# Kernel optimization log

Measured on AMD Instinct MI355X. Metric: run time of the kernel, lower is better.

## Reference

```python
import jax, jax.numpy as jnp
import numpy as np

B, C, H, W = 8, 320, 64, 64
NUM_SAMPLES = 3


def _skew(v):
    z = jnp.zeros((), v.dtype)
    return jnp.stack([
        jnp.stack([z, -v[2], v[1]]),
        jnp.stack([v[2], z, -v[0]]),
        jnp.stack([-v[1], v[0], z]),
    ])


def _rodrigues(rv):
    theta = jnp.linalg.norm(rv)
    r = rv / jnp.maximum(theta, 1e-12)
    I = jnp.eye(3, dtype=rv.dtype)
    R = jnp.cos(theta) * I + (1 - jnp.cos(theta)) * jnp.outer(r, r) + jnp.sin(theta) * _skew(r)
    return jnp.where(theta < 1e-6, I, R)


def _fundamental(Ks, Kt, ps, pt):
    Rs = jax.vmap(_rodrigues)(ps[:, :3])
    Rt = jax.vmap(_rodrigues)(pt[:, :3])
    ts, tt = ps[:, 3:], pt[:, 3:]
    R_rel = jnp.einsum('bij,bkj->bik', Rs, Rt)          # R_s @ R_t^T
    t_rel = ts - jnp.einsum('bij,bj->bi', R_rel, tt)
    E = jnp.einsum('bij,bjk->bik', jax.vmap(_skew)(t_rel), R_rel)
    inv_Ks = jnp.linalg.inv(Ks)
    inv_Kt = jnp.linalg.inv(Kt)
    return jnp.einsum('bji,bjk,bkl->bil', inv_Kt, E, inv_Ks)  # inv(Kt)^T @ E @ inv(Ks)


def _epipolar_warp(x, Ks, Kt, ps, pt, conv_w, conv_b):
    Bs, Cc, Hh, Ww = x.shape
    Fm = _fundamental(Ks, Kt, ps, pt)
    # pixel homogeneous coords, row-major flatten; H==W makes torch's i*H+j
    # loop index identical to this flat order
    k = jnp.arange(Hh * Ww)
    px = (k % Ww).astype(x.dtype)
    py = (k // Ww).astype(x.dtype)
    P = jnp.stack([px, py, jnp.ones_like(px)])            # [3, HW]
    lines = jnp.einsum('bji,jn->bin', Fm, P)              # F^T @ P -> [B,3,HW]
    a, b, c = lines[:, 0], lines[:, 1], lines[:, 2]
    W1, H1 = float(Ww - 1), float(Hh - 1)
    EPS = 1e-10
    x1 = jnp.clip(-c / (a + EPS), 0.0, W1)
    x2 = jnp.clip(-(b * H1 + c) / (a + EPS), 0.0, W1)
    y1 = jnp.clip(-c / (b + EPS), 0.0, H1)
    y2 = jnp.clip(-(a * W1 + c) / (b + EPS), 0.0, H1)
    t = jnp.linspace(0.0, 1.0, NUM_SAMPLES, dtype=x.dtype)
    sx = (x1[..., None] * (1 - t) + x2[..., None] * t).reshape(Bs, -1)  # [B, HW*3]
    sy = (y1[..., None] * (1 - t) + y2[..., None] * t).reshape(Bs, -1)
    # bilinear sampling; grid_sample(align_corners=True) normalization round-trips
    # back to pixel coords, and all samples are in-bounds by construction
    x0 = jnp.floor(sx)
    y0 = jnp.floor(sy)
    wx = sx - x0
    wy = sy - y0
    x0i = jnp.clip(x0, 0, Ww - 1).astype(jnp.int32)
    x1i = jnp.clip(x0 + 1, 0, Ww - 1).astype(jnp.int32)
    y0i = jnp.clip(y0, 0, Hh - 1).astype(jnp.int32)
    y1i = jnp.clip(y0 + 1, 0, Hh - 1).astype(jnp.int32)
    flat = x.reshape(Bs, Cc, Hh * Ww)

    def gather(yi, xi):
        return jnp.take_along_axis(flat, (yi * Ww + xi)[:, None, :], axis=2)  # [B,C,HW*3]

    g00, g10 = gather(y0i, x0i), gather(y0i, x1i)
    g01, g11 = gather(y1i, x0i), gather(y1i, x1i)
    wx_, wy_ = wx[:, None], wy[:, None]
    val = (g00 * (1 - wx_) * (1 - wy_) + g10 * wx_ * (1 - wy_)
           + g01 * (1 - wx_) * wy_ + g11 * wx_ * wy_)
    sampled = val.reshape(Bs, Cc, Hh * Ww, NUM_SAMPLES).mean(-1).reshape(Bs, Cc, Hh, Ww)
    out = jax.lax.conv_general_dilated(sampled, conv_w, (1, 1), 'SAME',
                                       dimension_numbers=('NCHW', 'OIHW', 'NCHW'))
    out = out + conv_b[None, :, None, None]
    return jax.nn.relu(out)


def setup_inputs() -> dict:
    key = jax.random.key(0)
    ks = jax.random.split(key, 8)
    x = jax.random.normal(ks[0], (B, C, H, W), dtype=jnp.float32)

    def make_K(kk):
        f = jax.random.uniform(kk, (B,), minval=400.0, maxval=600.0, dtype=jnp.float32)
        K = jnp.zeros((B, 3, 3), jnp.float32)
        K = K.at[:, 0, 0].set(f).at[:, 1, 1].set(f)
        K = K.at[:, 0, 2].set(W / 2.0).at[:, 1, 2].set(H / 2.0).at[:, 2, 2].set(1.0)
        return K

    source_intrinsics = make_K(ks[1])
    target_intrinsics = make_K(ks[2])
    source_pose = jnp.concatenate([
        0.3 * jax.random.normal(ks[3], (B, 3), jnp.float32),
        jax.random.normal(ks[4], (B, 3), jnp.float32)], axis=1)
    target_pose = jnp.concatenate([
        0.3 * jax.random.normal(ks[5], (B, 3), jnp.float32),
        jax.random.normal(ks[6], (B, 3), jnp.float32)], axis=1)
    fan_in = C * 3 * 3
    conv_w = jax.random.normal(ks[7], (C, C, 3, 3), jnp.float32) / np.sqrt(fan_in)
    conv_b = jnp.zeros((C,), jnp.float32)
    return {"x": x, "source_intrinsics": source_intrinsics,
            "target_intrinsics": target_intrinsics, "source_pose": source_pose,
            "target_pose": target_pose, "conv_w": conv_w, "conv_b": conv_b}


def reference(x, source_intrinsics, target_intrinsics, source_pose, target_pose, conv_w, conv_b):
    return _epipolar_warp(x, source_intrinsics, target_intrinsics,
                          source_pose, target_pose, conv_w, conv_b)
```

## Files before the change

kernel.cpp:

```cpp
#include <hip/hip_runtime.h>
#include <math.h>

#define BATCH 8
#define CH 320
#define HW 4096

typedef unsigned short u16;
typedef __attribute__((ext_vector_type(8))) short bf16x8;
typedef __attribute__((ext_vector_type(8))) unsigned short u16x8;
typedef __attribute__((ext_vector_type(4))) float f32x4;
typedef __attribute__((ext_vector_type(4))) float float4v;

#define ZP_OFF 0
#define SAMP_OFF 788480
#define WT_OFF 21760000

#define IBUF_BYTES 17408
#define A_OFF (2*IBUF_BYTES)
#define APHASE 61440
#define LDS_TOTAL (A_OFF + 2*APHASE)

__device__ __forceinline__ u16 f2bf(float f) {
    union { float f; unsigned u; } v; v.f = f;
    unsigned r = v.u + 0x7fffu + ((v.u >> 16) & 1u);
    return (u16)(r >> 16);
}
__device__ __forceinline__ float bf2f(u16 h) {
    union { unsigned u; float f; } v; v.u = ((unsigned)h) << 16;
    return v.f;
}
__device__ __forceinline__ void gl_lds16(const void* g, void* l) {
    __builtin_amdgcn_global_load_lds(
        (const __attribute__((address_space(1))) unsigned*)g,
        (__attribute__((address_space(3))) unsigned*)l, 16, 0, 0);
}

__device__ __forceinline__ void rodrigues3(float rv0, float rv1, float rv2, float* R) {
    float theta = sqrtf(rv0*rv0 + rv1*rv1 + rv2*rv2);
    float it = 1.0f / fmaxf(theta, 1e-12f);
    float r0 = rv0*it, r1 = rv1*it, r2 = rv2*it;
    float c = cosf(theta), s = sinf(theta), o = 1.0f - c;
    R[0]=c+o*r0*r0;    R[1]=o*r0*r1-s*r2; R[2]=o*r0*r2+s*r1;
    R[3]=o*r1*r0+s*r2; R[4]=c+o*r1*r1;    R[5]=o*r1*r2-s*r0;
    R[6]=o*r2*r0-s*r1; R[7]=o*r2*r1+s*r0; R[8]=c+o*r2*r2;
    if (theta < 1e-6f) { R[0]=1;R[1]=0;R[2]=0;R[3]=0;R[4]=1;R[5]=0;R[6]=0;R[7]=0;R[8]=1; }
}

__device__ __forceinline__ void inv3(const float* M, float* o) {
    float a=M[0],b=M[1],c=M[2],d=M[3],e=M[4],f=M[5],g=M[6],h=M[7],i=M[8];
    float A = e*i - f*h, B = f*g - d*i, C = d*h - e*g;
    float id = 1.0f / (a*A + b*B + c*C);
    o[0]=A*id;         o[1]=(c*h-b*i)*id; o[2]=(b*f-c*e)*id;
    o[3]=B*id;         o[4]=(a*i-c*g)*id; o[5]=(c*d-a*f)*id;
    o[6]=C*id;         o[7]=(b*g-a*h)*id; o[8]=(a*e-b*d)*id;
}

__device__ void compute_F(const float* Ks, const float* Kt, const float* ps,
                          const float* pt, int b, float* Fm) {
    float Rs[9], Rt[9];
    rodrigues3(ps[b*6+0], ps[b*6+1], ps[b*6+2], Rs);
    rodrigues3(pt[b*6+0], pt[b*6+1], pt[b*6+2], Rt);
    float Rr[9];
    #pragma unroll
    for (int i = 0; i < 3; ++i)
      #pragma unroll
      for (int k = 0; k < 3; ++k)
        Rr[i*3+k] = Rs[i*3+0]*Rt[k*3+0] + Rs[i*3+1]*Rt[k*3+1] + Rs[i*3+2]*Rt[k*3+2];
    float tt0 = pt[b*6+3], tt1 = pt[b*6+4], tt2 = pt[b*6+5];
    float tr0 = ps[b*6+3] - (Rr[0]*tt0 + Rr[1]*tt1 + Rr[2]*tt2);
    float tr1 = ps[b*6+4] - (Rr[3]*tt0 + Rr[4]*tt1 + Rr[5]*tt2);
    float tr2 = ps[b*6+5] - (Rr[6]*tt0 + Rr[7]*tt1 + Rr[8]*tt2);
    float E[9];
    #pragma unroll
    for (int j = 0; j < 3; ++j) {
        E[0*3+j] = -tr2*Rr[1*3+j] + tr1*Rr[2*3+j];
        E[1*3+j] =  tr2*Rr[0*3+j] - tr0*Rr[2*3+j];
        E[2*3+j] = -tr1*Rr[0*3+j] + tr0*Rr[1*3+j];
    }
    float iKs[9], iKt[9];
    inv3(Ks + b*9, iKs);
    inv3(Kt + b*9, iKt);
    float T[9];
    #pragma unroll
    for (int i = 0; i < 3; ++i)
      #pragma unroll
      for (int k = 0; k < 3; ++k)
        T[i*3+k] = iKt[0*3+i]*E[0*3+k] + iKt[1*3+i]*E[1*3+k] + iKt[2*3+i]*E[2*3+k];
    #pragma unroll
    for (int i = 0; i < 3; ++i)
      #pragma unroll
      for (int l = 0; l < 3; ++l)
        Fm[i*3 + l] = T[i*3+0]*iKs[0*3+l] + T[i*3+1]*iKs[1*3+l] + T[i*3+2]*iKs[2*3+l];
}

#define PLIDX(p) (((p)<<3) ^ (((p)&0x70)>>1))

__global__ __launch_bounds__(512) void k_sample8(const float* __restrict__ x,
                                                 const float* __restrict__ Ks,
                                                 const float* __restrict__ Kt,
                                                 const float* __restrict__ ps,
                                                 const float* __restrict__ pt,
                                                 const float* __restrict__ wsrc,
                                                 u16* __restrict__ wt,
                                                 float* __restrict__ zp,
                                                 u16* __restrict__ st) {
    __shared__ u16 pl[HW*8];
    int cg = blockIdx.x, b = blockIdx.y;
    int tid = threadIdx.x;
    int bid = b*40 + cg;

    for (int e = bid*512 + tid; e < 9*CH*CH; e += 320*512) {
        int cl = e & 31;
        int r  = e >> 5;
        int co = r % CH;
        int q  = r / CH;
        int t  = q % 9;
        int cc = q / 9;
        int ci = cc*32 + cl;
        wt[e] = f2bf(wsrc[((size_t)co*CH + ci)*9 + t]);
    }
    if (bid == 0 && tid < 256) zp[tid] = 0.0f;

    const float* xb = x + ((size_t)b*CH + cg*8)*HW;
    const float4v* xb4 = (const float4v*)xb;
    #pragma unroll
    for (int it = 0; it < 2; ++it) {
        int i0 = (it*512 + tid)*4;
        float4v v[8];
        #pragma unroll
        for (int c = 0; c < 8; ++c) v[c] = xb4[c*(HW/4) + it*512 + tid];
        #pragma unroll
        for (int j = 0; j < 4; ++j) {
            u16x8 o;
            #pragma unroll
            for (int c = 0; c < 8; ++c) o[c] = f2bf(v[c][j]);
            int pix = i0 + j;
            *(u16x8*)(pl + PLIDX(pix)) = o;
        }
    }
    float Fm[9];
    compute_F(Ks, Kt, ps, pt, b, Fm);
    __syncthreads();
    const float EPS = 1e-10f, W1 = 63.0f, H1 = 63.0f;
    u16* ob = st + ((size_t)bid)*HW*8;
    for (int k = tid; k < HW; k += 512) {
        float px = (float)(k & 63);
        float py = (float)(k >> 6);
        float a  = Fm[0]*px + Fm[3]*py + Fm[6];
        float bb = Fm[1]*px + Fm[4]*py + Fm[7];
        float c  = Fm[2]*px + Fm[5]*py + Fm[8];
        float x1 = fminf(fmaxf(-c/(a+EPS), 0.0f), W1);
        float x2 = fminf(fmaxf(-(bb*H1+c)/(a+EPS), 0.0f), W1);
        float y1 = fminf(fmaxf(-c/(bb+EPS), 0.0f), H1);
        float y2 = fminf(fmaxf(-(a*W1+c)/(bb+EPS), 0.0f), H1);
        float sxs[3], sys[3];
        sxs[0] = x1; sys[0] = y1;
        sxs[1] = 0.5f*(x1+x2); sys[1] = 0.5f*(y1+y2);
        sxs[2] = x2; sys[2] = y2;
        float acc[8];
        #pragma unroll
        for (int c2 = 0; c2 < 8; ++c2) acc[c2] = 0.f;
        #pragma unroll
        for (int s = 0; s < 3; ++s) {
            float sx = sxs[s], sy = sys[s];
            float fx = floorf(sx), fy = floorf(sy);
            float wx = sx-fx, wy = sy-fy;
            int x0 = (int)fx, y0 = (int)fy;
            int x1i = min(x0+1,63), y1i = min(y0+1,63);
            u16x8 g00 = *(const u16x8*)(pl + PLIDX(y0*64+x0));
            u16x8 g10 = *(const u16x8*)(pl + PLIDX(y0*64+x1i));
            u16x8 g01 = *(const u16x8*)(pl + PLIDX(y1i*64+x0));
            u16x8 g11 = *(const u16x8*)(pl + PLIDX(y1i*64+x1i));
            float w00=(1.f-wx)*(1.f-wy), w10=wx*(1.f-wy), w01=(1.f-wx)*wy, w11=wx*wy;
            #pragma unroll
            for (int c2 = 0; c2 < 8; ++c2)
                acc[c2] += w00*bf2f(g00[c2]) + w10*bf2f(g10[c2])
                         + w01*bf2f(g01[c2]) + w11*bf2f(g11[c2]);
        }
        u16x8 o;
        #pragma unroll
        for (int c2 = 0; c2 < 8; ++c2) o[c2] = f2bf(acc[c2]*(1.f/3.f));
        *(u16x8*)(ob + (size_t)k*8) = o;
    }
}

__global__ __launch_bounds__(512, 1) void k_conv(const u16* __restrict__ st,
                                                 const u16* __restrict__ wt,
                                                 const float* __restrict__ bias,
                                                 const float* __restrict__ zp,
                                                 float* __restrict__ out) {
    __shared__ __align__(16) char lds[LDS_TOTAL];
    int bid = blockIdx.x;
    int b      = bid & 7;
    int rowblk = bid >> 3;
    int y0 = rowblk*2;
    int lane = threadIdx.x & 63;
    int w = threadIdx.x >> 6;
    int wrow = w & 1;
    int co0w = (w >> 1) * 80;
    int l15 = lane & 15, l4 = lane >> 4;

    const u16* ga[3];
    int js[3], stp[3];
    #pragma unroll
    for (int s = 0; s < 3; ++s) {
        int j = (s < 2) ? (s*8 + w) : 16;
        js[s] = j;
        int g = j*64 + lane;
        int row_l = g/264;
        int rem = g - row_l*264;
        int col = rem >> 2;
        int slot = rem & 3;
        int ks = slot ^ ((col>>1)&3);
        int yy = y0 - 1 + row_l;
        int xx = col - 1;
        bool oob = (g >= 1056) | (yy < 0) | (yy > 63) | (xx < 0) | (xx > 63);
        int yc = min(max(yy,0),63), xc = min(max(xx,0),63);
        const u16* p = st + (((size_t)b*40 + ks)*HW + (yc*64 + xc))*8;
        ga[s]  = oob ? (const u16*)zp : p;
        stp[s] = oob ? 0 : 4*HW*8;
    }
    int nslot = (w == 0) ? 3 : 2;

    int alaneoff = ((lane>>2)<<6) + ((((lane&3) ^ ((lane>>3)&3))) << 4);
    const char* asrc = (const char*)wt + alaneoff;

    int ard_off = (co0w + l15)*64 + ((l4 ^ ((l15>>1)&3)) << 4);

    f32x4 acc[5][4];
    #pragma unroll
    for (int mr = 0; mr < 5; ++mr)
        #pragma unroll
        for (int nf = 0; nf < 4; ++nf) acc[mr][nf] = (f32x4){0.f,0.f,0.f,0.f};

    #pragma unroll
    for (int s = 0; s < 3; ++s)
        if (s < nslot) gl_lds16(ga[s], lds + js[s]*1024);
    #pragma unroll
    for (int s = 0; s < 3; ++s) ga[s] += stp[s];
    #pragma unroll
    for (int s = 0; s < 8; ++s) {
        int j = s*8 + w;
        if (j < 60) gl_lds16(asrc + j*1024, lds + A_OFF + j*1024);
    }
    asrc += APHASE;
    __syncthreads();

    for (int c = 0; c < 10; ++c) {
        const char* ibuf = lds + (c&1)*IBUF_BYTES;
        #pragma unroll
        for (int ky = 0; ky < 3; ++ky) {
            int p = c*3 + ky;
            if (p < 29) {
                char* adst = lds + A_OFF + ((p+1)&1)*APHASE;
                #pragma unroll
                for (int s = 0; s < 8; ++s) {
                    int j = s*8 + w;
                    if (j < 60) gl_lds16(asrc + j*1024, adst + j*1024);
                }
                asrc += APHASE;
            }
            if (ky == 0 && c < 9) {
                char* idst = lds + ((c&1)^1)*IBUF_BYTES;
                #pragma unroll
                for (int s = 0; s < 3; ++s)
                    if (s < nslot) gl_lds16(ga[s], idst + js[s]*1024);
                #pragma unroll
                for (int s = 0; s < 3; ++s) ga[s] += stp[s];
            }
            const char* abuf = lds + A_OFF + (p&1)*APHASE;
            int rowbase = (wrow + ky) * 4224;
            #pragma unroll
            for (int kx = 0; kx < 3; ++kx) {
                bf16x8 bb[4];
                #pragma unroll
                for (int nf = 0; nf < 4; ++nf) {
                    int col = nf*16 + l15 + kx;
                    int boff = rowbase + col*64 + ((l4 ^ ((col>>1)&3))<<4);
                    bb[nf] = *(const bf16x8*)(ibuf + boff);
                }
                bf16x8 a[5];
                #pragma unroll
                for (int mr = 0; mr < 5; ++mr)
                    a[mr] = *(const bf16x8*)(abuf + kx*20480 + mr*1024 + ard_off);
                #pragma unroll
                for (int mr = 0; mr < 5; ++mr)
                    #pragma unroll
                    for (int nf = 0; nf < 4; ++nf)
                        acc[mr][nf] = __builtin_amdgcn_mfma_f32_16x16x32_bf16(
                            a[mr], bb[nf], acc[mr][nf], 0, 0, 0);
            }
            __syncthreads();
        }
    }

    int y = y0 + wrow;
    #pragma unroll
    for (int mr = 0; mr < 5; ++mr) {
        #pragma unroll
        for (int r = 0; r < 4; ++r) {
            int co = co0w + mr*16 + l4*4 + r;
            float bv = bias[co];
            float* ob = out + ((size_t)(b*CH + co))*HW + y*64;
            #pragma unroll
            for (int nf = 0; nf < 4; ++nf) {
                int xx = nf*16 + l15;
                ob[xx] = fmaxf(acc[mr][nf][r] + bv, 0.f);
            }
        }
    }
}

extern "C" void kernel_launch(void* const* d_in, const int* in_sizes, int n_in,
                              void* d_out, int out_size, void* d_ws, size_t ws_size,
                              hipStream_t stream) {
    const float* x  = (const float*)d_in[0];
    const float* Ks = (const float*)d_in[1];
    const float* Kt = (const float*)d_in[2];
    const float* ps = (const float*)d_in[3];
    const float* pt = (const float*)d_in[4];
    const float* cw = (const float*)d_in[5];
    const float* cb = (const float*)d_in[6];
    float* out = (float*)d_out;
    char* ws = (char*)d_ws;
    float* zp = (float*)(ws + ZP_OFF);
    u16*   st = (u16*)(ws + SAMP_OFF);
    u16*   wt = (u16*)(ws + WT_OFF);

    k_sample8<<<dim3(CH/8, BATCH), 512, 0, stream>>>(x, Ks, Kt, ps, pt, cw, wt, zp, st);
    k_conv<<<256, 512, 0, stream>>>(st, wt, cb, zp, out);
}
```

Measured before the change: 87.22 us.

## Load conv weight fragments directly to registers with double-buffered prefetch

The conv GEMM's weight (A) operand is no longer staged through LDS. Each wave loads its fragments straight from global memory into registers with inline-asm dwordx4 loads, double-buffered across the 9 kernel taps. Waits on explicit vmcnt counters replace most barriers, keeping only one per input chunk. This drops the LDS traffic and the per-tap syncthreads for weights, and shrinks LDS use, which may allow more blocks per CU. In exchange it needs more registers and more redundant global and L2 reads of the weights across waves, and the hand-counted vmcnt values are fragile.

```diff
diff --git a/kernel.cpp b/kernel.cpp
--- a/kernel.cpp
+++ b/kernel.cpp
@@ -16,9 +16,10 @@
 #define WT_OFF 21760000
 
 #define IBUF_BYTES 17408
-#define A_OFF (2*IBUF_BYTES)
-#define APHASE 61440
-#define LDS_TOTAL (A_OFF + 2*APHASE)
+#define LDS_TOTAL (2*IBUF_BYTES)
+
+#define WAITV(N) asm volatile("s_waitcnt vmcnt(" #N ")" ::: "memory")
+#define ALD(d, p_) asm volatile("global_load_dwordx4 %0, %1, off" : "=v"(d) : "v"(p_) : "memory")
 
 __device__ __forceinline__ u16 f2bf(float f) {
     union { float f; unsigned u; } v; v.f = f;
@@ -222,76 +223,87 @@
     }
     int nslot = (w == 0) ? 3 : 2;
 
-    int alaneoff = ((lane>>2)<<6) + ((((lane&3) ^ ((lane>>3)&3))) << 4);
-    const char* asrc = (const char*)wt + alaneoff;
-
-    int ard_off = (co0w + l15)*64 + ((l4 ^ ((l15>>1)&3)) << 4);
+    int awoff = (co0w + l15)*32 + l4*8;
+    const u16* ap0 = wt + awoff + 0*512;
+    const u16* ap1 = wt + awoff + 1*512;
+    const u16* ap2 = wt + awoff + 2*512;
+    const u16* ap3 = wt + awoff + 3*512;
+    const u16* ap4 = wt + awoff + 4*512;
 
     f32x4 acc[5][4];
     #pragma unroll
     for (int mr = 0; mr < 5; ++mr)
         #pragma unroll
         for (int nf = 0; nf < 4; ++nf) acc[mr][nf] = (f32x4){0.f,0.f,0.f,0.f};
+
+    bf16x8 aA[5], aB[5];
 
     #pragma unroll
     for (int s = 0; s < 3; ++s)
         if (s < nslot) gl_lds16(ga[s], lds + js[s]*1024);
     #pragma unroll
     for (int s = 0; s < 3; ++s) ga[s] += stp[s];
-    #pragma unroll
-    for (int s = 0; s < 8; ++s) {
-        int j = s*8 + w;
-        if (j < 60) gl_lds16(asrc + j*1024, lds + A_OFF + j*1024);
-    }
-    asrc += APHASE;
-    __syncthreads();
-
-    for (int c = 0; c < 10; ++c) {
-        const char* ibuf = lds + (c&1)*IBUF_BYTES;
-        #pragma unroll
-        for (int ky = 0; ky < 3; ++ky) {
-            int p = c*3 + ky;
-            if (p < 29) {
-                char* adst = lds + A_OFF + ((p+1)&1)*APHASE;
-                #pragma unroll
-                for (int s = 0; s < 8; ++s) {
-                    int j = s*8 + w;
-                    if (j < 60) gl_lds16(asrc + j*1024, adst + j*1024);
-                }
-                asrc += APHASE;
-            }
-            if (ky == 0 && c < 9) {
-                char* idst = lds + ((c&1)^1)*IBUF_BYTES;
-                #pragma unroll
-                for (int s = 0; s < 3; ++s)
-                    if (s < nslot) gl_lds16(ga[s], idst + js[s]*1024);
-                #pragma unroll
-                for (int s = 0; s < 3; ++s) ga[s] += stp[s];
-            }
-            const char* abuf = lds + A_OFF + (p&1)*APHASE;
-            int rowbase = (wrow + ky) * 4224;
-            #pragma unroll
-            for (int kx = 0; kx < 3; ++kx) {
-                bf16x8 bb[4];
-                #pragma unroll
-                for (int nf = 0; nf < 4; ++nf) {
-                    int col = nf*16 + l15 + kx;
-                    int boff = rowbase + col*64 + ((l4 ^ ((col>>1)&3))<<4);
-                    bb[nf] = *(const bf16x8*)(ibuf + boff);
-                }
-                bf16x8 a[5];
-                #pragma unroll
-                for (int mr = 0; mr < 5; ++mr)
-                    a[mr] = *(const bf16x8*)(abuf + kx*20480 + mr*1024 + ard_off);
-                #pragma unroll
-                for (int mr = 0; mr < 5; ++mr)
-                    #pragma unroll
-                    for (int nf = 0; nf < 4; ++nf)
-                        acc[mr][nf] = __builtin_amdgcn_mfma_f32_16x16x32_bf16(
-                            a[mr], bb[nf], acc[mr][nf], 0, 0, 0);
-            }
-            __syncthreads();
-        }
+    ALD(aA[0], ap0); ALD(aA[1], ap1); ALD(aA[2], ap2); ALD(aA[3], ap3); ALD(aA[4], ap4);
+    ap0 += 10240; ap1 += 10240; ap2 += 10240; ap3 += 10240; ap4 += 10240;
+    WAITV(0);
+    __builtin_amdgcn_s_barrier();
+
+#define STEP(c_, t_, AU, AN) do {                                              \
+    bool last_ = ((c_) == 9) && ((t_) == 8);                                   \
+    if (!last_) {                                                              \
+        ALD(AN[0], ap0); ALD(AN[1], ap1); ALD(AN[2], ap2);                     \
+        ALD(AN[3], ap3); ALD(AN[4], ap4);                                      \
+        ap0 += 10240; ap1 += 10240; ap2 += 10240; ap3 += 10240; ap4 += 10240;  \
+    }                                                                          \
+    if ((t_) == 0 && (c_) < 9) {                                               \
+        char* idst_ = lds + (((c_)&1)^1)*IBUF_BYTES;                           \
+        _Pragma("unroll")                                                      \
+        for (int s_ = 0; s_ < 3; ++s_)                                         \
+            if (s_ < nslot) gl_lds16(ga[s_], idst_ + js[s_]*1024);             \
+        _Pragma("unroll")                                                      \
+        for (int s_ = 0; s_ < 3; ++s_) ga[s_] += stp[s_];                      \
+        if (w == 0) { WAITV(8); } else { WAITV(7); }                           \
+    } else if (!last_) { WAITV(5); } else { WAITV(0); }                        \
+    __builtin_amdgcn_sched_barrier(0);                                         \
+    {                                                                          \
+        const char* ibuf_ = lds + ((c_)&1)*IBUF_BYTES;                         \
+        const int ky_ = (t_)/3, kx_ = (t_)%3;                                  \
+        int rowbase_ = (wrow + ky_) * 4224;                                    \
+        bf16x8 bb_[4];                                                         \
+        _Pragma("unroll")                                                      \
+        for (int nf = 0; nf < 4; ++nf) {                                       \
+            int col = nf*16 + l15 + kx_;                                       \
+            int boff = rowbase_ + col*64 + ((l4 ^ ((col>>1)&3))<<4);           \
+            bb_[nf] = *(const bf16x8*)(ibuf_ + boff);                          \
+        }                                                                      \
+        _Pragma("unroll")                                                      \
+        for (int mr = 0; mr < 5; ++mr)                                         \
+            _Pragma("unroll")                                                  \
+            for (int nf = 0; nf < 4; ++nf)                                     \
+                acc[mr][nf] = __builtin_amdgcn_mfma_f32_16x16x32_bf16(         \
+                    AU[mr], bb_[nf], acc[mr][nf], 0, 0, 0);                    \
+    }                                                                          \
+} while (0)
+
+#define CHUNK_P0(c_) do {                                                      \
+    STEP(c_,0,aA,aB); STEP(c_,1,aB,aA); STEP(c_,2,aA,aB);                      \
+    STEP(c_,3,aB,aA); STEP(c_,4,aA,aB); STEP(c_,5,aB,aA);                      \
+    STEP(c_,6,aA,aB); STEP(c_,7,aB,aA); STEP(c_,8,aA,aB);                      \
+    asm volatile("s_waitcnt lgkmcnt(0)" ::: "memory");                         \
+    __builtin_amdgcn_s_barrier();                                              \
+} while (0)
+#define CHUNK_P1(c_) do {                                                      \
+    STEP(c_,0,aB,aA); STEP(c_,1,aA,aB); STEP(c_,2,aB,aA);                      \
+    STEP(c_,3,aA,aB); STEP(c_,4,aB,aA); STEP(c_,5,aA,aB);                      \
+    STEP(c_,6,aB,aA); STEP(c_,7,aA,aB); STEP(c_,8,aB,aA);                      \
+    asm volatile("s_waitcnt lgkmcnt(0)" ::: "memory");                         \
+    __builtin_amdgcn_s_barrier();                                              \
+} while (0)
+
+    for (int cc = 0; cc < 5; ++cc) {
+        int c0 = 2*cc, c1 = 2*cc + 1;
+        CHUNK_P0(c0);
+        CHUNK_P1(c1);
     }
 
     int y = y0 + wrow;
```

After: 98.59 us. 1.13x slower.
